# Optimization experiments

Measured on AMD Instinct MI355X. Metric: run time of the kernel, lower is better.

The kernel has to match this reference:

```python
import jax, jax.numpy as jnp
import numpy as np

TEMP = 0.2
N_IT = 10
P = 1


def setup_inputs() -> dict:
    key = jax.random.key(0)
    N, M = 8192, 8192
    cdist = jax.random.uniform(key, (N, M), dtype=jnp.float32)
    A = jnp.ones((N,), dtype=jnp.float32) / N
    B = jnp.ones((M,), dtype=jnp.float32) / M
    return {"cdist": cdist, "A": A, "B": B}


def _sinkhorn(cdist, A, B):
    # torch .std() is the unbiased (ddof=1) std over all elements
    n = cdist.size
    std = jnp.sqrt(jnp.var(cdist) * (n / (n - 1)))
    c = cdist / std
    c = c - jnp.min(c)
    C = c if P == 1 else c ** P
    Q = jnp.exp(-C / TEMP)
    Q = Q / jnp.sum(Q)

    def body(i, T):
        T = T * (B / jnp.sum(T, axis=0))          # match column marginal B
        T = T * (A / jnp.sum(T, axis=1))[:, None]  # match row marginal A
        return T

    return jax.lax.fori_loop(0, N_IT, body, Q)


def reference(cdist, A, B):
    return _sinkhorn(cdist, A, B)
```

## Files before the change

kernel.cpp:

```cpp
#include <hip/hip_runtime.h>
#include <hip/hip_bf16.h>

#define TEMP_ 0.2f

static constexpr int RPC = 32;

__device__ __forceinline__ float blo(unsigned int u){ return __uint_as_float(u << 16); }
__device__ __forceinline__ float bhi(unsigned int u){ return __uint_as_float(u & 0xFFFF0000u); }
__device__ __forceinline__ unsigned int pack2(float a, float b){
    unsigned int ua = __float_as_uint(a), ub = __float_as_uint(b);
    ua += 0x7FFFu + ((ua >> 16) & 1u);
    ub += 0x7FFFu + ((ub >> 16) & 1u);
    return (ua >> 16) | (ub & 0xFFFF0000u);
}

__global__ void init_kernel(float* r, float* v, const float* __restrict__ Av, int N,
                            double* s, double* s2, int* mb){
    int i = blockIdx.x * blockDim.x + threadIdx.x;
    if (i < N){ r[i] = 1.0f; v[i] = Av[i]; }
    if (i == 0){ *s = 0.0; *s2 = 0.0; *mb = 0x7F800000; }
}

__global__ void stats_kernel(const float* __restrict__ x, long long n4,
                             double* s, double* s2, int* mb){
    long long i = blockIdx.x * (long long)blockDim.x + threadIdx.x;
    long long stride = (long long)gridDim.x * blockDim.x;
    const float4* x4 = (const float4*)x;
    double a = 0.0, b = 0.0;
    float mn = __int_as_float(0x7F800000);
    for (; i < n4; i += stride){
        float4 v = x4[i];
        a += (double)v.x + (double)v.y + (double)v.z + (double)v.w;
        b += (double)v.x * v.x + (double)v.y * v.y + (double)v.z * v.z + (double)v.w * v.w;
        mn = fminf(mn, fminf(fminf(v.x, v.y), fminf(v.z, v.w)));
    }
    #pragma unroll
    for (int off = 32; off; off >>= 1){
        a  += __shfl_down(a, off);
        b  += __shfl_down(b, off);
        mn  = fminf(mn, __shfl_down(mn, off));
    }
    __shared__ double sa[4], sb[4]; __shared__ float sm[4];
    int w = threadIdx.x >> 6, l = threadIdx.x & 63;
    if (l == 0){ sa[w] = a; sb[w] = b; sm[w] = mn; }
    __syncthreads();
    if (threadIdx.x == 0){
        int nw = blockDim.x >> 6;
        for (int k = 1; k < nw; ++k){ a += sa[k]; b += sb[k]; mn = fminf(mn, sm[k]); }
        atomicAdd(s, a);
        atomicAdd(s2, b);
        atomicMin(mb, __float_as_int(mn));
    }
}

__global__ void finalize_kernel(const double* s, const double* s2, const int* mb,
                                double n, float* coefs){
    double mean = *s / n;
    double var  = *s2 / n - mean * mean;
    double stdv = sqrt(var * (n / (n - 1.0)));
    coefs[0] = (float)(1.0 / (stdv * (double)TEMP_));
    coefs[1] = __int_as_float(*mb);
}

__global__ void build_q_kernel(const float* __restrict__ x, unsigned int* __restrict__ q,
                               const float* __restrict__ coefs, long long n){
    float a = coefs[0], mv = coefs[1];
    long long i = (blockIdx.x * (long long)blockDim.x + threadIdx.x) * 8;
    if (i >= n) return;
    float4 v0 = *(const float4*)(x + i);
    float4 v1 = *(const float4*)(x + i + 4);
    float q0 = __expf((mv - v0.x) * a), q1 = __expf((mv - v0.y) * a);
    float q2 = __expf((mv - v0.z) * a), q3 = __expf((mv - v0.w) * a);
    float q4 = __expf((mv - v1.x) * a), q5 = __expf((mv - v1.y) * a);
    float q6 = __expf((mv - v1.z) * a), q7 = __expf((mv - v1.w) * a);
    uint4 o;
    o.x = pack2(q0, q1); o.y = pack2(q2, q3); o.z = pack2(q4, q5); o.w = pack2(q6, q7);
    *(uint4*)(q + (i >> 1)) = o;
}

template<int MODE>
__global__ __launch_bounds__(1024)
void gstep2_kernel(const unsigned int* __restrict__ qg,
                   const float* __restrict__ Av,
                   const float* __restrict__ cg,
                   float* __restrict__ P,
                   float* __restrict__ r)
{
    constexpr int FM  = 8192;
    constexpr int RU4 = FM / 8;
    constexpr int SU4 = 4 * RU4;
    extern __shared__ uint4 lds4[];
    __shared__ float sv[16];

    const int tid  = threadIdx.x;
    const int b    = blockIdx.x;
    const int w    = tid >> 6, lane = tid & 63;
    const uint4* g4 = (const uint4*)qg + (long long)b * 8 * SU4;

    {
        uint4 p0 = g4[tid], p1 = g4[tid + 1024], p2 = g4[tid + 2048], p3 = g4[tid + 3072];
        lds4[tid] = p0; lds4[tid + 1024] = p1; lds4[tid + 2048] = p2; lds4[tid + 3072] = p3;
    }
    __syncthreads();

    float acc[8] = {0,0,0,0,0,0,0,0};

    for (int s = 0; s < 8; ++s){
        const uint4* cur = lds4 + (s & 1) * SU4;
        uint4*       nxt = lds4 + ((s + 1) & 1) * SU4;
        uint4 p0, p1, p2, p3;
        const bool pf = (s + 1 < 8);
        if (pf){
            const uint4* gn = g4 + (long long)(s + 1) * SU4;
            p0 = gn[tid]; p1 = gn[tid + 1024]; p2 = gn[tid + 2048]; p3 = gn[tid + 3072];
        }

        float rv0 = 1.f, rv1 = 1.f, rv2 = 1.f, rv3 = 1.f;
        if (MODE != 0){
            int row = w >> 2, quar = w & 3;
            const uint4* lr = cur + row * RU4 + quar * 256;
            float a1 = 0.f;
            #pragma unroll
            for (int k = 0; k < 4; ++k){
                uint4 qq = lr[lane + k * 64];
                int j = (quar * 256 + lane + k * 64) * 8;
                float4 c0 = *(const float4*)(cg + j);
                float4 c1 = *(const float4*)(cg + j + 4);
                a1 += blo(qq.x)*c0.x + bhi(qq.x)*c0.y + blo(qq.y)*c0.z + bhi(qq.y)*c0.w
                    + blo(qq.z)*c1.x + bhi(qq.z)*c1.y + blo(qq.w)*c1.z + bhi(qq.w)*c1.w;
            }
            #pragma unroll
            for (int off = 32; off; off >>= 1) a1 += __shfl_down(a1, off);
            if (lane == 0) sv[w] = a1;
            asm volatile("s_waitcnt lgkmcnt(0)" ::: "memory");
            __builtin_amdgcn_s_barrier();
            __builtin_amdgcn_sched_barrier(0);
            const float* Ab = Av + b * 32 + s * 4;
            rv0 = Ab[0] / (sv[0]  + sv[1]  + sv[2]  + sv[3]);
            rv1 = Ab[1] / (sv[4]  + sv[5]  + sv[6]  + sv[7]);
            rv2 = Ab[2] / (sv[8]  + sv[9]  + sv[10] + sv[11]);
            rv3 = Ab[3] / (sv[12] + sv[13] + sv[14] + sv[15]);
            if (MODE == 2 && tid < 4){
                float rr = (tid == 0) ? rv0 : (tid == 1) ? rv1 : (tid == 2) ? rv2 : rv3;
                r[b * 32 + s * 4 + tid] = rr;
            }
        }

        if (MODE != 2){
            uint4 q0 = cur[tid];
            uint4 q1 = cur[RU4 + tid];
            uint4 q2 = cur[2 * RU4 + tid];
            uint4 q3 = cur[3 * RU4 + tid];
            acc[0] += rv0*blo(q0.x) + rv1*blo(q1.x) + rv2*blo(q2.x) + rv3*blo(q3.x);
            acc[1] += rv0*bhi(q0.x) + rv1*bhi(q1.x) + rv2*bhi(q2.x) + rv3*bhi(q3.x);
            acc[2] += rv0*blo(q0.y) + rv1*blo(q1.y) + rv2*blo(q2.y) + rv3*blo(q3.y);
            acc[3] += rv0*bhi(q0.y) + rv1*bhi(q1.y) + rv2*bhi(q2.y) + rv3*bhi(q3.y);
            acc[4] += rv0*blo(q0.z) + rv1*blo(q1.z) + rv2*blo(q2.z) + rv3*blo(q3.z);
            acc[5] += rv0*bhi(q0.z) + rv1*bhi(q1.z) + rv2*bhi(q2.z) + rv3*bhi(q3.z);
            acc[6] += rv0*blo(q0.w) + rv1*blo(q1.w) + rv2*blo(q2.w) + rv3*blo(q3.w);
            acc[7] += rv0*bhi(q0.w) + rv1*bhi(q1.w) + rv2*bhi(q2.w) + rv3*bhi(q3.w);
        }

        __syncthreads();
        if (pf){
            nxt[tid] = p0; nxt[tid + 1024] = p1; nxt[tid + 2048] = p2; nxt[tid + 3072] = p3;
            __syncthreads();
        }
    }

    if (MODE != 2){
        float* Pr = P + (long long)b * FM + tid * 8;
        *(float4*)(Pr)     = make_float4(acc[0], acc[1], acc[2], acc[3]);
        *(float4*)(Pr + 4) = make_float4(acc[4], acc[5], acc[6], acc[7]);
    }
}

__global__ __launch_bounds__(1024)
void colfin2_kernel(const float* __restrict__ Bv, const float* __restrict__ P,
                    float* __restrict__ c, int M, int RC){
    __shared__ float red[1024];
    int col = blockIdx.x * 64 + (threadIdx.x & 63);
    int w   = threadIdx.x >> 6;
    float s = 0.f;
    for (int k = w; k < RC; k += 16)
        s += P[(long long)k * M + col];
    red[threadIdx.x] = s;
    __syncthreads();
    if (w == 0){
        float t = 0.f;
        #pragma unroll
        for (int g = 0; g < 16; ++g) t += red[(threadIdx.x & 63) + 64 * g];
        c[col] = Bv[col] / t;
    }
}

template<bool USE_Q>
__global__ void colsum_kernel(const unsigned int* __restrict__ q, const float* __restrict__ x,
                              const float* __restrict__ coefs, const float* __restrict__ r,
                              float* __restrict__ P, int M){
    int j0   = blockIdx.x * 2048 + threadIdx.x * 8;
    int row0 = blockIdx.y * RPC;
    float a = 0.f, mv = 0.f;
    if (!USE_Q){ a = coefs[0]; mv = coefs[1]; }
    float acc[8] = {0,0,0,0,0,0,0,0};
    for (int it = 0; it < RPC; ++it){
        int row = row0 + it;
        float rv = r[row];
        long long base = (long long)row * M + j0;
        if (USE_Q){
            uint4 qq = *(const uint4*)(q + (base >> 1));
            acc[0] += rv * blo(qq.x); acc[1] += rv * bhi(qq.x);
            acc[2] += rv * blo(qq.y); acc[3] += rv * bhi(qq.y);
            acc[4] += rv * blo(qq.z); acc[5] += rv * bhi(qq.z);
            acc[6] += rv * blo(qq.w); acc[7] += rv * bhi(qq.w);
        } else {
            float4 v0 = *(const float4*)(x + base);
            float4 v1 = *(const float4*)(x + base + 4);
            acc[0] += rv * __expf((mv - v0.x) * a); acc[1] += rv * __expf((mv - v0.y) * a);
            acc[2] += rv * __expf((mv - v0.z) * a); acc[3] += rv * __expf((mv - v0.w) * a);
            acc[4] += rv * __expf((mv - v1.x) * a); acc[5] += rv * __expf((mv - v1.y) * a);
            acc[6] += rv * __expf((mv - v1.z) * a); acc[7] += rv * __expf((mv - v1.w) * a);
        }
    }
    float* Pr = P + (long long)blockIdx.y * M + j0;
    *(float4*)(Pr)     = make_float4(acc[0], acc[1], acc[2], acc[3]);
    *(float4*)(Pr + 4) = make_float4(acc[4], acc[5], acc[6], acc[7]);
}

__global__ void colfin_kernel(const float* __restrict__ Bv, const float* __restrict__ P,
                              float* __restrict__ c, int M, int RC){
    int j = blockIdx.x * blockDim.x + threadIdx.x;
    if (j >= M) return;
    float s = 0.f;
    for (int rc = 0; rc < RC; ++rc) s += P[(long long)rc * M + j];
    c[j] = Bv[j] / s;
}

template<bool USE_Q>
__global__ void rowsum_kernel(const unsigned int* __restrict__ q, const float* __restrict__ x,
                              const float* __restrict__ coefs, const float* __restrict__ c,
                              float* __restrict__ v, int M){
    int gid  = blockIdx.x * blockDim.x + threadIdx.x;
    int row  = gid >> 6;
    int lane = gid & 63;
    float a = 0.f, mv = 0.f;
    if (!USE_Q){ a = coefs[0]; mv = coefs[1]; }
    long long base = (long long)row * M;
    float acc = 0.f;
    for (int j = lane * 8; j < M; j += 512){
        float4 c0 = *(const float4*)(c + j);
        float4 c1 = *(const float4*)(c + j + 4);
        if (USE_Q){
            uint4 qq = *(const uint4*)(q + ((base + j) >> 1));
            acc += blo(qq.x) * c0.x + bhi(qq.x) * c0.y + blo(qq.y) * c0.z + bhi(qq.y) * c0.w
                 + blo(qq.z) * c1.x + bhi(qq.z) * c1.y + blo(qq.w) * c1.z + bhi(qq.w) * c1.w;
        } else {
            float4 v0 = *(const float4*)(x + base + j);
            float4 v1 = *(const float4*)(x + base + j + 4);
            acc += __expf((mv - v0.x) * a) * c0.x + __expf((mv - v0.y) * a) * c0.y
                 + __expf((mv - v0.z) * a) * c0.z + __expf((mv - v0.w) * a) * c0.w
                 + __expf((mv - v1.x) * a) * c1.x + __expf((mv - v1.y) * a) * c1.y
                 + __expf((mv - v1.z) * a) * c1.z + __expf((mv - v1.w) * a) * c1.w;
        }
    }
    #pragma unroll
    for (int off = 32; off; off >>= 1) acc += __shfl_down(acc, off);
    if (lane == 0) v[row] = acc;
}

__global__ void rowfin_kernel(const float* __restrict__ Av, const float* __restrict__ vv,
                              float* __restrict__ r, int N){
    int i = blockIdx.x * blockDim.x + threadIdx.x;
    if (i < N) r[i] = Av[i] / vv[i];
}

__global__ void final_kernel(const float* __restrict__ x, const float* __restrict__ coefs,
                             const float* __restrict__ r, const float* __restrict__ c,
                             float* __restrict__ out, int M){
    long long i = (blockIdx.x * (long long)blockDim.x + threadIdx.x) * 4;
    int row = (int)(i / M);
    int j   = (int)(i - (long long)row * M);
    float a = coefs[0], mv = coefs[1];
    float rv = r[row];
    float4 v  = *(const float4*)(x + i);
    float4 cc = *(const float4*)(c + j);
    float4 o;
    o.x = rv * cc.x * __expf((mv - v.x) * a);
    o.y = rv * cc.y * __expf((mv - v.y) * a);
    o.z = rv * cc.z * __expf((mv - v.z) * a);
    o.w = rv * cc.w * __expf((mv - v.w) * a);
    *(float4*)(out + i) = o;
}

extern "C" void kernel_launch(void* const* d_in, const int* in_sizes, int n_in,
                              void* d_out, int out_size, void* d_ws, size_t ws_size,
                              hipStream_t stream){
    const float* x  = (const float*)d_in[0];
    const float* Av = (const float*)d_in[1];
    const float* Bv = (const float*)d_in[2];
    float* out = (float*)d_out;
    int N = in_sizes[1], M = in_sizes[2];
    long long NM = (long long)N * M;

    char* ws = (char*)d_ws;
    double* s    = (double*)(ws + 0);
    double* s2   = (double*)(ws + 8);
    int*    mb   = (int*)   (ws + 16);
    float*  coefs= (float*) (ws + 24);
    size_t off = 64;
    float* v = (float*)(ws + off); off += (size_t)N * 4;
    float* r = (float*)(ws + off); off += (size_t)N * 4;
    float* c = (float*)(ws + off); off += (size_t)M * 4;
    int RC = N / RPC;
    float* P = (float*)(ws + off); off += (size_t)RC * M * 4;
    off = (off + 255) & ~(size_t)255;
    unsigned int* q = (unsigned int*)(ws + off);
    const bool use_q = (ws_size >= off + (size_t)NM * 2);

    static int s_attr = -1;
    if (s_attr < 0){
        hipError_t e0 = hipFuncSetAttribute(reinterpret_cast<const void*>(gstep2_kernel<0>),
                                            hipFuncAttributeMaxDynamicSharedMemorySize, 131072);
        hipError_t e1 = hipFuncSetAttribute(reinterpret_cast<const void*>(gstep2_kernel<1>),
                                            hipFuncAttributeMaxDynamicSharedMemorySize, 131072);
        hipError_t e2 = hipFuncSetAttribute(reinterpret_cast<const void*>(gstep2_kernel<2>),
                                            hipFuncAttributeMaxDynamicSharedMemorySize, 131072);
        s_attr = (e0 == hipSuccess && e1 == hipSuccess && e2 == hipSuccess) ? 1 : 0;
    }
    const bool fast = use_q && s_attr == 1 && (M == 8192) && (N % 32 == 0);

    init_kernel<<<(N + 255) / 256, 256, 0, stream>>>(r, v, Av, N, s, s2, mb);
    stats_kernel<<<2048, 256, 0, stream>>>(x, NM >> 2, s, s2, mb);
    finalize_kernel<<<1, 1, 0, stream>>>(s, s2, mb, (double)NM, coefs);

    if (fast){
        const size_t ldsB = 131072;
        build_q_kernel<<<(int)(NM / 8 / 256), 256, 0, stream>>>(x, q, coefs, NM);
        gstep2_kernel<0><<<N / 32, 1024, ldsB, stream>>>(q, Av, c, P, r);
        for (int t = 1; t <= 10; ++t){
            colfin2_kernel<<<M / 64, 1024, 0, stream>>>(Bv, P, c, M, RC);
            if (t < 10) gstep2_kernel<1><<<N / 32, 1024, ldsB, stream>>>(q, Av, c, P, r);
            else        gstep2_kernel<2><<<N / 32, 1024, ldsB, stream>>>(q, Av, c, P, r);
        }
    } else if (use_q){
        build_q_kernel<<<(int)(NM / 8 / 256), 256, 0, stream>>>(x, q, coefs, NM);
        dim3 cgrid(M / 2048, RC);
        int rgrid = N / 4;
        for (int it = 0; it < 10; ++it){
            colsum_kernel<true ><<<cgrid, 256, 0, stream>>>(q, x, coefs, r, P, M);
            colfin_kernel<<<(M + 255) / 256, 256, 0, stream>>>(Bv, P, c, M, RC);
            rowsum_kernel<true ><<<rgrid, 256, 0, stream>>>(q, x, coefs, c, v, M);
            rowfin_kernel<<<(N + 255) / 256, 256, 0, stream>>>(Av, v, r, N);
        }
    } else {
        dim3 cgrid(M / 2048, RC);
        int rgrid = N / 4;
        for (int it = 0; it < 10; ++it){
            colsum_kernel<false><<<cgrid, 256, 0, stream>>>(q, x, coefs, r, P, M);
            colfin_kernel<<<(M + 255) / 256, 256, 0, stream>>>(Bv, P, c, M, RC);
            rowsum_kernel<false><<<rgrid, 256, 0, stream>>>(q, x, coefs, c, v, M);
            rowfin_kernel<<<(N + 255) / 256, 256, 0, stream>>>(Av, v, r, N);
        }
    }

    final_kernel<<<(int)(NM / 4 / 256), 256, 0, stream>>>(x, coefs, r, c, out, M);
}
```

Before: 952.9 us.

## Fuse Q construction into first step and stream Q through registers instead of LDS

The first sweep now builds the bf16 Q matrix and its per-block column partial sums in one kernel, so the separate build pass and its re-read of Q go away. The iterative step kernel drops the 128 KB LDS staging and keeps each thread's column slice of Q in registers with a two-stage register double buffer. Each thread also loads its slice of the column scaling once and computes four row dot products at a time, using one barrier per step instead of three. This trades LDS traffic and synchronisation for higher register pressure and direct global loads.

Result: slower. 3.622 ms (+280.1%).

```diff
diff --git a/kernel.cpp b/kernel.cpp
--- a/kernel.cpp
+++ b/kernel.cpp
@@ -80,77 +80,100 @@
 
 template<int MODE>
 __global__ __launch_bounds__(1024)
-void gstep2_kernel(const unsigned int* __restrict__ qg,
+void gstep3_kernel(const unsigned int* __restrict__ qg,
+                   const float* __restrict__ xg,
+                   const float* __restrict__ coefs,
                    const float* __restrict__ Av,
                    const float* __restrict__ cg,
                    float* __restrict__ P,
+                   unsigned int* __restrict__ qout,
                    float* __restrict__ r)
 {
-    constexpr int FM  = 8192;
-    constexpr int RU4 = FM / 8;
-    constexpr int SU4 = 4 * RU4;
-    extern __shared__ uint4 lds4[];
-    __shared__ float sv[16];
-
-    const int tid  = threadIdx.x;
-    const int b    = blockIdx.x;
-    const int w    = tid >> 6, lane = tid & 63;
-    const uint4* g4 = (const uint4*)qg + (long long)b * 8 * SU4;
-
-    {
-        uint4 p0 = g4[tid], p1 = g4[tid + 1024], p2 = g4[tid + 2048], p3 = g4[tid + 3072];
-        lds4[tid] = p0; lds4[tid + 1024] = p1; lds4[tid + 2048] = p2; lds4[tid + 3072] = p3;
-    }
-    __syncthreads();
+    constexpr int RU4 = 1024;
+    __shared__ float sv[2][4][16];
+    const int tid = threadIdx.x, b = blockIdx.x;
+    const int w = tid >> 6, lane = tid & 63;
 
     float acc[8] = {0,0,0,0,0,0,0,0};
 
+    if (MODE == 0){
+        float a = coefs[0], mv = coefs[1];
+        const float4* x4 = (const float4*)xg + (long long)b * 32 * 2048 + tid * 2;
+        uint4* q4 = (uint4*)qout + (long long)b * 32 * RU4 + tid;
+        #pragma unroll 4
+        for (int row = 0; row < 32; ++row){
+            float4 v0 = x4[(long long)row * 2048];
+            float4 v1 = x4[(long long)row * 2048 + 1];
+            uint4 o;
+            o.x = pack2(__expf((mv - v0.x) * a), __expf((mv - v0.y) * a));
+            o.y = pack2(__expf((mv - v0.z) * a), __expf((mv - v0.w) * a));
+            o.z = pack2(__expf((mv - v1.x) * a), __expf((mv - v1.y) * a));
+            o.w = pack2(__expf((mv - v1.z) * a), __expf((mv - v1.w) * a));
+            q4[(long long)row * RU4] = o;
+            acc[0] += blo(o.x); acc[1] += bhi(o.x); acc[2] += blo(o.y); acc[3] += bhi(o.y);
+            acc[4] += blo(o.z); acc[5] += bhi(o.z); acc[6] += blo(o.w); acc[7] += bhi(o.w);
+        }
+        float* Pr = P + (long long)b * 8192 + tid * 8;
+        *(float4*)(Pr)     = make_float4(acc[0], acc[1], acc[2], acc[3]);
+        *(float4*)(Pr + 4) = make_float4(acc[4], acc[5], acc[6], acc[7]);
+        return;
+    }
+
+    const uint4* g4 = (const uint4*)qg + (long long)b * 32 * RU4 + tid;
+    float4 cv0 = *(const float4*)(cg + tid * 8);
+    float4 cv1 = *(const float4*)(cg + tid * 8 + 4);
+
+    uint4 buf[2][4];
+    #pragma unroll
+    for (int rr = 0; rr < 4; ++rr) buf[0][rr] = g4[rr * RU4];
+
+    #pragma unroll
     for (int s = 0; s < 8; ++s){
-        const uint4* cur = lds4 + (s & 1) * SU4;
-        uint4*       nxt = lds4 + ((s + 1) & 1) * SU4;
-        uint4 p0, p1, p2, p3;
-        const bool pf = (s + 1 < 8);
-        if (pf){
-            const uint4* gn = g4 + (long long)(s + 1) * SU4;
-            p0 = gn[tid]; p1 = gn[tid + 1024]; p2 = gn[tid + 2048]; p3 = gn[tid + 3072];
-        }
-
-        float rv0 = 1.f, rv1 = 1.f, rv2 = 1.f, rv3 = 1.f;
-        if (MODE != 0){
-            int row = w >> 2, quar = w & 3;
-            const uint4* lr = cur + row * RU4 + quar * 256;
-            float a1 = 0.f;
+        const int cur = s & 1, nxt = cur ^ 1;
+        if (s < 7){
             #pragma unroll
-            for (int k = 0; k < 4; ++k){
-                uint4 qq = lr[lane + k * 64];
-                int j = (quar * 256 + lane + k * 64) * 8;
-                float4 c0 = *(const float4*)(cg + j);
-                float4 c1 = *(const float4*)(cg + j + 4);
-                a1 += blo(qq.x)*c0.x + bhi(qq.x)*c0.y + blo(qq.y)*c0.z + bhi(qq.y)*c0.w
-                    + blo(qq.z)*c1.x + bhi(qq.z)*c1.y + blo(qq.w)*c1.z + bhi(qq.w)*c1.w;
+            for (int rr = 0; rr < 4; ++rr) buf[nxt][rr] = g4[((s + 1) * 4 + rr) * RU4];
+        }
+        float4 av4 = *(const float4*)(Av + b * 32 + s * 4);
+
+        float d[4];
+        #pragma unroll
+        for (int rr = 0; rr < 4; ++rr){
+            uint4 qq = buf[cur][rr];
+            d[rr] = blo(qq.x)*cv0.x + bhi(qq.x)*cv0.y + blo(qq.y)*cv0.z + bhi(qq.y)*cv0.w
+                  + blo(qq.z)*cv1.x + bhi(qq.z)*cv1.y + blo(qq.w)*cv1.z + bhi(qq.w)*cv1.w;
+        }
+        #pragma unroll
+        for (int off = 32; off; off >>= 1){
+            d[0] += __shfl_down(d[0], off); d[1] += __shfl_down(d[1], off);
+            d[2] += __shfl_down(d[2], off); d[3] += __shfl_down(d[3], off);
+        }
+        if (lane == 0){
+            sv[cur][0][w] = d[0]; sv[cur][1][w] = d[1];
+            sv[cur][2][w] = d[2]; sv[cur][3][w] = d[3];
+        }
+        asm volatile("s_waitcnt lgkmcnt(0)\n\ts_barrier" ::: "memory");
+
+        float vr[4];
+        #pragma unroll
+        for (int rr = 0; rr < 4; ++rr){
+            float4 a0 = *(const float4*)(&sv[cur][rr][0]);
+            float4 a1 = *(const float4*)(&sv[cur][rr][4]);
+            float4 a2 = *(const float4*)(&sv[cur][rr][8]);
+            float4 a3 = *(const float4*)(&sv[cur][rr][12]);
+            vr[rr] = (a0.x + a0.y + a0.z + a0.w) + (a1.x + a1.y + a1.z + a1.w)
+                   + (a2.x + a2.y + a2.z + a2.w) + (a3.x + a3.y + a3.z + a3.w);
+        }
+        float rv0 = av4.x / vr[0], rv1 = av4.y / vr[1];
+        float rv2 = av4.z / vr[2], rv3 = av4.w / vr[3];
+
+        if (MODE == 2){
+            if (tid < 4){
+                float rr_ = (tid == 0) ? rv0 : (tid == 1) ? rv1 : (tid == 2) ? rv2 : rv3;
+                r[b * 32 + s * 4 + tid] = rr_;
             }
-            #pragma unroll
-            for (int off = 32; off; off >>= 1) a1 += __shfl_down(a1, off);
-            if (lane == 0) sv[w] = a1;
-            asm volatile("s_waitcnt lgkmcnt(0)" ::: "memory");
-            __builtin_amdgcn_s_barrier();
-            __builtin_amdgcn_sched_barrier(0);
-            const float* Ab = Av + b * 32 + s * 4;
-            rv0 = Ab[0] / (sv[0]  + sv[1]  + sv[2]  + sv[3]);
-            rv1 = Ab[1] / (sv[4]  + sv[5]  + sv[6]  + sv[7]);
-            rv2 = Ab[2] / (sv[8]  + sv[9]  + sv[10] + sv[11]);
-            rv3 = Ab[3] / (sv[12] + sv[13] + sv[14] + sv[15]);
-            if (MODE == 2 && tid < 4){
-                float rr = (tid == 0) ? rv0 : (tid == 1) ? rv1 : (tid == 2) ? rv2 : rv3;
-                r[b * 32 + s * 4 + tid] = rr;
-            }
-        }
-
-        if (MODE != 2){
-            uint4 q0 = cur[tid];
-            uint4 q1 = cur[RU4 + tid];
-            uint4 q2 = cur[2 * RU4 + tid];
-            uint4 q3 = cur[3 * RU4 + tid];
+        } else {
+            uint4 q0 = buf[cur][0], q1 = buf[cur][1], q2 = buf[cur][2], q3 = buf[cur][3];
             acc[0] += rv0*blo(q0.x) + rv1*blo(q1.x) + rv2*blo(q2.x) + rv3*blo(q3.x);
             acc[1] += rv0*bhi(q0.x) + rv1*bhi(q1.x) + rv2*bhi(q2.x) + rv3*bhi(q3.x);
             acc[2] += rv0*blo(q0.y) + rv1*blo(q1.y) + rv2*blo(q2.y) + rv3*blo(q3.y);
@@ -160,16 +183,10 @@
             acc[6] += rv0*blo(q0.w) + rv1*blo(q1.w) + rv2*blo(q2.w) + rv3*blo(q3.w);
             acc[7] += rv0*bhi(q0.w) + rv1*bhi(q1.w) + rv2*bhi(q2.w) + rv3*bhi(q3.w);
         }
-
-        __syncthreads();
-        if (pf){
-            nxt[tid] = p0; nxt[tid + 1024] = p1; nxt[tid + 2048] = p2; nxt[tid + 3072] = p3;
-            __syncthreads();
-        }
-    }
-
-    if (MODE != 2){
-        float* Pr = P + (long long)b * FM + tid * 8;
+    }
+
+    if (MODE == 1){
+        float* Pr = P + (long long)b * 8192 + tid * 8;
         *(float4*)(Pr)     = make_float4(acc[0], acc[1], acc[2], acc[3]);
         *(float4*)(Pr + 4) = make_float4(acc[4], acc[5], acc[6], acc[7]);
     }
@@ -317,30 +334,18 @@
     unsigned int* q = (unsigned int*)(ws + off);
     const bool use_q = (ws_size >= off + (size_t)NM * 2);
 
-    static int s_attr = -1;
-    if (s_attr < 0){
-        hipError_t e0 = hipFuncSetAttribute(reinterpret_cast<const void*>(gstep2_kernel<0>),
-                                            hipFuncAttributeMaxDynamicSharedMemorySize, 131072);
-        hipError_t e1 = hipFuncSetAttribute(reinterpret_cast<const void*>(gstep2_kernel<1>),
-                                            hipFuncAttributeMaxDynamicSharedMemorySize, 131072);
-        hipError_t e2 = hipFuncSetAttribute(reinterpret_cast<const void*>(gstep2_kernel<2>),
-                                            hipFuncAttributeMaxDynamicSharedMemorySize, 131072);
-        s_attr = (e0 == hipSuccess && e1 == hipSuccess && e2 == hipSuccess) ? 1 : 0;
-    }
-    const bool fast = use_q && s_attr == 1 && (M == 8192) && (N % 32 == 0);
+    const bool fast = use_q && (M == 8192) && (N % 32 == 0);
 
     init_kernel<<<(N + 255) / 256, 256, 0, stream>>>(r, v, Av, N, s, s2, mb);
     stats_kernel<<<2048, 256, 0, stream>>>(x, NM >> 2, s, s2, mb);
     finalize_kernel<<<1, 1, 0, stream>>>(s, s2, mb, (double)NM, coefs);
 
     if (fast){
-        const size_t ldsB = 131072;
-        build_q_kernel<<<(int)(NM / 8 / 256), 256, 0, stream>>>(x, q, coefs, NM);
-        gstep2_kernel<0><<<N / 32, 1024, ldsB, stream>>>(q, Av, c, P, r);
+        gstep3_kernel<0><<<N / 32, 1024, 0, stream>>>(q, x, coefs, Av, c, P, q, r);
         for (int t = 1; t <= 10; ++t){
             colfin2_kernel<<<M / 64, 1024, 0, stream>>>(Bv, P, c, M, RC);
-            if (t < 10) gstep2_kernel<1><<<N / 32, 1024, ldsB, stream>>>(q, Av, c, P, r);
-            else        gstep2_kernel<2><<<N / 32, 1024, ldsB, stream>>>(q, Av, c, P, r);
+            if (t < 10) gstep3_kernel<1><<<N / 32, 1024, 0, stream>>>(q, x, coefs, Av, c, P, q, r);
+            else        gstep3_kernel<2><<<N / 32, 1024, 0, stream>>>(q, x, coefs, Av, c, P, q, r);
         }
     } else if (use_q){
         build_q_kernel<<<(int)(NM / 8 / 256), 256, 0, stream>>>(x, q, coefs, NM);
```
